# Performance work log

Hardware: AMD Instinct MI355X
Metric: run time of the kernel (lower is better)

Reference implementation:

```python
import jax, jax.numpy as jnp
import numpy as np
from jax import lax


def setup_inputs() -> dict:
    key = jax.random.key(0)
    ks = jax.random.split(key, 6)
    B, C, H, W = 8, 128, 64, 64   # C = 2*channel, channel (per-branch) c = 64
    c = C // 2
    return {
        "x_up": jax.random.normal(ks[0], (B, C, H, W), dtype=jnp.float32),
        "x_skip": jax.random.normal(ks[1], (B, C, H, W), dtype=jnp.float32),
        # nn.Linear(c, 2c): weight [out,in], bias [out]
        "kv1_w": jax.random.normal(ks[2], (2 * c, c), dtype=jnp.float32) * 0.05,
        "kv1_b": jnp.zeros((2 * c,), dtype=jnp.float32),
        "kv2_w": jax.random.normal(ks[3], (2 * c, c), dtype=jnp.float32) * 0.05,
        "kv2_b": jnp.zeros((2 * c,), dtype=jnp.float32),
        # Conv2d(2c, 2c, 3, stride 1, pad 1, bias=False), OIHW
        "conv_w": jax.random.normal(ks[4], (C, C, 3, 3), dtype=jnp.float32) * 0.05,
        # BatchNorm2d(2c) in inference form (running stats)
        "bn_gamma": jax.random.normal(ks[5], (C,), dtype=jnp.float32) * 0.1 + 1.0,
        "bn_beta": jnp.zeros((C,), dtype=jnp.float32),
        "bn_mean": jnp.zeros((C,), dtype=jnp.float32),
        "bn_var": jnp.ones((C,), dtype=jnp.float32),
    }


def reference(x_up, x_skip, kv1_w, kv1_b, kv2_w, kv2_b, conv_w,
              bn_gamma, bn_beta, bn_mean, bn_var):
    b, C, h, w = x_up.shape
    c = C // 2
    hw = h * w
    up1, up2 = x_up[:, :c], x_up[:, c:]
    sk1, sk2 = x_skip[:, :c], x_skip[:, c:]

    # ---- spatial attention branch (softmax over last axis, hw x hw) ----
    shortcut1 = up1 + sk1
    u1 = up1.reshape(b, c, hw).transpose(0, 2, 1)   # (b, hw, c)
    s1 = sk1.reshape(b, c, hw).transpose(0, 2, 1)   # (b, hw, c)
    kv = s1 @ kv1_w.T + kv1_b                        # (b, hw, 2c)
    k1, v1 = kv[..., :c], kv[..., c:]
    attn = jax.nn.softmax(jnp.einsum('bnc,bmc->bnm', u1, k1), axis=-1)  # (b, hw, hw)
    sout = jnp.einsum('bnm,bmc->bnc', attn, v1)      # (b, hw, c)
    sout = sout.transpose(0, 2, 1).reshape(b, c, h, w) + shortcut1

    # ---- channel attention branch (softmax over dim=1 of the c x c map) ----
    shortcut2 = up2 + sk2
    u2 = up2.reshape(b, c, hw).transpose(0, 2, 1)    # (b, hw, c)
    s2 = sk2.reshape(b, c, hw).transpose(0, 2, 1)
    kv = s2 @ kv2_w.T + kv2_b                        # (b, hw, 2c)
    k2, v2 = kv[..., :c], kv[..., c:]
    A = jax.nn.softmax(jnp.einsum('bnc,bnd->bcd', u2, k2), axis=1)  # (b, c, c)
    cout = jnp.einsum('bnc,bcd->bnd', v2, A)          # (b, hw, c)
    cout = cout.transpose(0, 2, 1).reshape(b, c, h, w) + shortcut2

    # ---- conv + BN (inference) + ReLU ----
    x = jnp.concatenate([sout, cout], axis=1)         # (b, 2c, h, w)
    y = lax.conv_general_dilated(x, conv_w, (1, 1), 'SAME',
                                 dimension_numbers=('NCHW', 'OIHW', 'NCHW'))
    inv = jax.lax.rsqrt(bn_var + 1e-5)
    y = (y - bn_mean[None, :, None, None]) * (inv * bn_gamma)[None, :, None, None] \
        + bn_beta[None, :, None, None]
    return jax.nn.relu(y)
```

## Files before the change

### kernel.cpp

```cpp
#include <hip/hip_runtime.h>
#include <math.h>

#define HW 4096

typedef __attribute__((ext_vector_type(8))) short bh8;
typedef __attribute__((ext_vector_type(4))) float f32x4;
typedef __attribute__((ext_vector_type(2))) unsigned int u32x2;
typedef unsigned int u32;
typedef unsigned short u16;

__device__ __forceinline__ u16 f2bf(float f) {
  union { float f; u32 u; } v; v.f = f;
  u32 u = v.u;
  return (u16)((u + 0x7FFFu + ((u >> 16) & 1u)) >> 16);
}
__device__ __forceinline__ float bf2f(u16 h) {
  union { u32 u; float f; } v; v.u = ((u32)h) << 16;
  return v.f;
}
__device__ __forceinline__ float ubits2f(u32 u) {
  union { u32 u; float f; } v; v.u = u;
  return v.f;
}
__device__ __forceinline__ u32 cvt_pk_bf16(float lo, float hi) {
  u32 r;
  asm("v_cvt_pk_bf16_f32 %0, %1, %2" : "=v"(r) : "v"(lo), "v"(hi));
  return r;
}
__device__ __forceinline__ float fexp2(float x) {
  float r;
  asm("v_exp_f32 %0, %1" : "=v"(r) : "v"(x));
  return r;
}

__global__ __launch_bounds__(256) void kv_proj(
    const float* __restrict__ xs,
    const float* __restrict__ w1, const float* __restrict__ b1,
    const float* __restrict__ w2, const float* __restrict__ b2,
    u32* __restrict__ Knm, u16* __restrict__ Vcm,
    u16* __restrict__ K2t, u16* __restrict__ V2t,
    const float* __restrict__ cw, const float* __restrict__ gamma,
    const float* __restrict__ beta, const float* __restrict__ mean,
    const float* __restrict__ var, u16* __restrict__ Wg,
    float* __restrict__ shb) {
  __shared__ __align__(16) u16 XsH[64][72];
  __shared__ __align__(16) u16 XsL[64][72];
  __shared__ u32 LtK[64][33];
  const int b = blockIdx.y, n0 = blockIdx.x * 64;
  const int t = threadIdx.x;
  const int wq = t >> 6, lane = t & 63, lq = lane & 15, quad = lane >> 4;
  const float* xsb = xs + (size_t)b * 128 * HW;

  {
    int gid = (blockIdx.y * 64 + blockIdx.x) * 256 + t;
    for (int i = gid; i < 147456; i += 131072) {
      int tap = i >> 14, oc = (i >> 7) & 127, ic = i & 127;
      float sc = gamma[oc] * rsqrtf(var[oc] + 1e-5f);
      Wg[i] = f2bf(cw[((size_t)(oc * 128 + ic)) * 9 + tap] * sc);
    }
    if (gid < 128) {
      float sc = gamma[gid] * rsqrtf(var[gid] + 1e-5f);
      shb[gid] = beta[gid] - mean[gid] * sc;
    }
  }

  for (int br = 0; br < 2; ++br) {
    const float* W = br ? w2 : w1;
    const float* bias = br ? b2 : b1;
    const float* src = xsb + (br ? 64 * HW : 0);

    bh8 wh[2][2], wl[2][2];
#pragma unroll
    for (int jt = 0; jt < 2; ++jt)
#pragma unroll
      for (int s = 0; s < 2; ++s) {
        const float* wr = W + (size_t)(wq * 32 + jt * 16 + lq) * 64 + s * 32 + quad * 8;
        float4 a0 = *(const float4*)wr;
        float4 a1 = *(const float4*)(wr + 4);
        float f[8] = {a0.x, a0.y, a0.z, a0.w, a1.x, a1.y, a1.z, a1.w};
        union { u32 u[4]; bh8 v; } H, L;
#pragma unroll
        for (int p = 0; p < 4; ++p) {
          u32 hp = cvt_pk_bf16(f[2 * p], f[2 * p + 1]);
          float h0 = ubits2f(hp << 16);
          float h1 = ubits2f(hp & 0xFFFF0000u);
          H.u[p] = hp;
          L.u[p] = cvt_pk_bf16(f[2 * p] - h0, f[2 * p + 1] - h1);
        }
        wh[jt][s] = H.v;
        wl[jt][s] = L.v;
      }

    if (br) __syncthreads();
    {
      const int n = t & 63, cg = t >> 6;
#pragma unroll
      for (int s8 = 0; s8 < 8; ++s8) {
        int ch0 = s8 * 8 + cg * 2;
        float f0 = src[(size_t)ch0 * HW + n0 + n];
        float f1 = src[(size_t)(ch0 + 1) * HW + n0 + n];
        u32 hp = cvt_pk_bf16(f0, f1);
        float h0 = ubits2f(hp << 16);
        float h1 = ubits2f(hp & 0xFFFF0000u);
        u32 lp = cvt_pk_bf16(f0 - h0, f1 - h1);
        *(u32*)&XsH[n][ch0] = hp;
        *(u32*)&XsL[n][ch0] = lp;
      }
    }
    __syncthreads();

    f32x4 acc[2][4];
#pragma unroll
    for (int nt = 0; nt < 4; ++nt) {
      const int xr = nt * 16 + lq;
      bh8 xh0 = *(const bh8*)&XsH[xr][quad * 8];
      bh8 xh1 = *(const bh8*)&XsH[xr][32 + quad * 8];
      bh8 xl0 = *(const bh8*)&XsL[xr][quad * 8];
      bh8 xl1 = *(const bh8*)&XsL[xr][32 + quad * 8];
#pragma unroll
      for (int jt = 0; jt < 2; ++jt) {
        f32x4 a = (f32x4)(0.f);
        a = __builtin_amdgcn_mfma_f32_16x16x32_bf16(wh[jt][0], xh0, a, 0, 0, 0);
        a = __builtin_amdgcn_mfma_f32_16x16x32_bf16(wh[jt][1], xh1, a, 0, 0, 0);
        a = __builtin_amdgcn_mfma_f32_16x16x32_bf16(wh[jt][0], xl0, a, 0, 0, 0);
        a = __builtin_amdgcn_mfma_f32_16x16x32_bf16(wh[jt][1], xl1, a, 0, 0, 0);
        a = __builtin_amdgcn_mfma_f32_16x16x32_bf16(wl[jt][0], xh0, a, 0, 0, 0);
        a = __builtin_amdgcn_mfma_f32_16x16x32_bf16(wl[jt][1], xh1, a, 0, 0, 0);
        acc[jt][nt] = a;
      }
    }

    if (br == 0) {
      if (wq < 2) {
#pragma unroll
        for (int jt = 0; jt < 2; ++jt) {
          float4 bv = *(const float4*)&bias[wq * 32 + jt * 16 + quad * 4];
#pragma unroll
          for (int nt = 0; nt < 4; ++nt) {
            f32x4 a = acc[jt][nt];
            LtK[nt * 16 + lq][wq * 16 + jt * 8 + quad * 2] =
                cvt_pk_bf16(a[0] + bv.x, a[1] + bv.y);
            LtK[nt * 16 + lq][wq * 16 + jt * 8 + quad * 2 + 1] =
                cvt_pk_bf16(a[2] + bv.z, a[3] + bv.w);
          }
        }
      } else {
#pragma unroll
        for (int jt = 0; jt < 2; ++jt) {
          float4 bv = *(const float4*)&bias[wq * 32 + jt * 16 + quad * 4];
          float bvv[4] = {bv.x, bv.y, bv.z, bv.w};
#pragma unroll
          for (int nt = 0; nt < 4; ++nt)
#pragma unroll
            for (int r = 0; r < 4; ++r) {
              int ch = (wq - 2) * 32 + jt * 16 + quad * 4 + r;
              Vcm[((size_t)b * 64 + ch) * HW + n0 + nt * 16 + lq] =
                  f2bf(acc[jt][nt][r] + bvv[r]);
            }
        }
      }
      __syncthreads();
#pragma unroll
      for (int p = 0; p < 8; ++p) {
        int idx = p * 256 + t;
        int n = idx >> 5, cc = idx & 31;
        Knm[((size_t)b * HW + n0 + n) * 32 + cc] = LtK[n][cc];
      }
    } else {
      u16* base = (wq < 2) ? (K2t + (size_t)b * 64 * HW) : (V2t + (size_t)b * 64 * HW);
      const int chb = (wq & 1) * 32;
#pragma unroll
      for (int jt = 0; jt < 2; ++jt) {
        float4 bv = *(const float4*)&bias[wq * 32 + jt * 16 + quad * 4];
        float bvv[4] = {bv.x, bv.y, bv.z, bv.w};
#pragma unroll
        for (int nt = 0; nt < 4; ++nt)
#pragma unroll
          for (int r = 0; r < 4; ++r) {
            int ch = chb + jt * 16 + quad * 4 + r;
            base[(size_t)ch * HW + n0 + nt * 16 + lq] =
                f2bf(acc[jt][nt][r] + bvv[r]);
          }
      }
    }
  }
}

__device__ __forceinline__ void attn_step(
    const bh8* kf, const bh8* vf, const bh8 (&qb)[4][2], const bh8 ones,
    f32x4 (&O)[4][4], f32x4 (&Osum)[4]) {
  f32x4 S[2][4];
  __builtin_amdgcn_s_setprio(1);
#pragma unroll
  for (int mt = 0; mt < 2; ++mt)
#pragma unroll
    for (int nt = 0; nt < 4; ++nt) {
      f32x4 a = (f32x4)(0.f);
      a = __builtin_amdgcn_mfma_f32_16x16x32_bf16(kf[mt * 2 + 0], qb[nt][0], a, 0, 0, 0);
      a = __builtin_amdgcn_mfma_f32_16x16x32_bf16(kf[mt * 2 + 1], qb[nt][1], a, 0, 0, 0);
      S[mt][nt] = a;
    }
  __builtin_amdgcn_s_setprio(0);
#pragma unroll
  for (int nt = 0; nt < 4; ++nt) {
    const float c = 17.312340f;
    float e00 = fexp2(S[0][nt][0] - c), e01 = fexp2(S[0][nt][1] - c);
    float e02 = fexp2(S[0][nt][2] - c), e03 = fexp2(S[0][nt][3] - c);
    float e10 = fexp2(S[1][nt][0] - c), e11 = fexp2(S[1][nt][1] - c);
    float e12 = fexp2(S[1][nt][2] - c), e13 = fexp2(S[1][nt][3] - c);
    u32 A = cvt_pk_bf16(e00, e01);
    u32 B = cvt_pk_bf16(e02, e03);
    u32 C = cvt_pk_bf16(e10, e11);
    u32 D = cvt_pk_bf16(e12, e13);
    u32x2 rac = __builtin_amdgcn_permlane32_swap(A, C, 0, 0);
    u32x2 rbd = __builtin_amdgcn_permlane32_swap(B, D, 0, 0);
    u32x2 r02 = __builtin_amdgcn_permlane16_swap(rac.x, rac.y, 0, 0);
    u32x2 r13 = __builtin_amdgcn_permlane16_swap(rbd.x, rbd.y, 0, 0);
    union { u32 u[4]; bh8 v; } pb;
    pb.u[0] = r02.x;
    pb.u[1] = r13.x;
    pb.u[2] = r02.y;
    pb.u[3] = r13.y;
    __builtin_amdgcn_s_setprio(1);
#pragma unroll
    for (int ct = 0; ct < 4; ++ct)
      O[ct][nt] = __builtin_amdgcn_mfma_f32_16x16x32_bf16(vf[ct], pb.v, O[ct][nt], 0, 0, 0);
    Osum[nt] = __builtin_amdgcn_mfma_f32_16x16x32_bf16(ones, pb.v, Osum[nt], 0, 0, 0);
    __builtin_amdgcn_s_setprio(0);
  }
}

#define LOADKV(KB, KF, VF)                                            \
  do {                                                                \
    const int n0_ = (KB) * 128;                                       \
    const u16* kr_ = Kb + (size_t)(n0_ + wb + lq) * 64 + quad * 8;    \
    KF[0] = *(const bh8*)(kr_);                                       \
    KF[1] = *(const bh8*)(kr_ + 32);                                  \
    KF[2] = *(const bh8*)(kr_ + 1024);                                \
    KF[3] = *(const bh8*)(kr_ + 1056);                                \
    const u16* vr_ = Vb + (size_t)lq * HW + n0_ + wb + quad * 8;      \
    VF[0] = *(const bh8*)(vr_);                                       \
    VF[1] = *(const bh8*)(vr_ + 16 * HW);                             \
    VF[2] = *(const bh8*)(vr_ + 32 * HW);                             \
    VF[3] = *(const bh8*)(vr_ + 48 * HW);                             \
  } while (0)

__global__ __launch_bounds__(256, 2) void attn_gram(
    const float* __restrict__ xu, const float* __restrict__ xs,
    const u16* __restrict__ Knm, const u16* __restrict__ Vcm,
    u16* __restrict__ xcat,
    const u16* __restrict__ K2t, float* __restrict__ Mp) {
  __shared__ __align__(16) u16 SMEM[18432];
  const int b = blockIdx.y;
  const int t = threadIdx.x;

  if (blockIdx.x >= 64) {
    float* Us = (float*)SMEM;
    float* Ksm = Us + 64 * 65;
    const int n0 = (blockIdx.x - 64) * 128;
    const int c = t & 63, dg = t >> 6;
    const float* ub = xu + ((size_t)b * 128 + 64) * HW;
    const u16* kb2 = K2t + (size_t)b * 64 * HW;
    float acc[16];
#pragma unroll
    for (int i = 0; i < 16; ++i) acc[i] = 0.f;
    for (int s = 0; s < 2; ++s) {
      int nn = n0 + s * 64;
      __syncthreads();
      for (int r = 0; r < 16; ++r) {
        int row = r * 4 + dg;
        Us[row * 65 + c] = ub[(size_t)row * HW + nn + c];
        Ksm[row * 65 + c] = bf2f(kb2[(size_t)row * HW + nn + c]);
      }
      __syncthreads();
      for (int n = 0; n < 64; ++n) {
        float u = Us[c * 65 + n];
#pragma unroll
        for (int i = 0; i < 16; ++i)
          acc[i] = fmaf(Ksm[(dg * 16 + i) * 65 + n], u, acc[i]);
      }
    }
    float* dst = Mp + ((size_t)(blockIdx.x - 64) * 8 + b) * 4096 + c * 64 + dg * 16;
#pragma unroll
    for (int i = 0; i < 16; ++i) dst[i] = acc[i];
    return;
  }

  const int q0 = blockIdx.x * 64;
  const int wq = t >> 6, lane = t & 63, lq = lane & 15, quad = lane >> 4;
  const int wb = wq * 32;
  const float* xub = xu + (size_t)b * 128 * HW;
  const float* xsb = xs + (size_t)b * 128 * HW;
  const u16* Kb = Knm + (size_t)b * HW * 64;
  const u16* Vb = Vcm + (size_t)b * 64 * HW;

  bh8 qb[4][2];
#pragma unroll
  for (int nt = 0; nt < 4; ++nt)
#pragma unroll
    for (int s = 0; s < 2; ++s)
#pragma unroll
      for (int j = 0; j < 8; ++j) {
        int ch = s * 32 + quad * 8 + j;
        qb[nt][s][j] =
            (short)f2bf(xub[(size_t)ch * HW + q0 + nt * 16 + lq] * 1.44269504f);
      }
  bh8 ones;
#pragma unroll
  for (int j = 0; j < 8; ++j) ones[j] = (short)0x3F80;

  f32x4 O[4][4];
#pragma unroll
  for (int ct = 0; ct < 4; ++ct)
#pragma unroll
    for (int nt = 0; nt < 4; ++nt) O[ct][nt] = (f32x4)(0.f);
  f32x4 Osum[4];
#pragma unroll
  for (int nt = 0; nt < 4; ++nt) Osum[nt] = (f32x4)(0.f);

  bh8 kfa[4], vfa[4], kfb[4], vfb[4];
  LOADKV(0, kfa, vfa);
  for (int kb = 0; kb < 32; kb += 2) {
    LOADKV(kb + 1, kfb, vfb);
    attn_step(kfa, vfa, qb, ones, O, Osum);
    if (kb + 2 < 32) LOADKV(kb + 2, kfa, vfa);
    attn_step(kfb, vfb, qb, ones, O, Osum);
  }

  float* Posc = (float*)SMEM;
  float* Lred = (float*)(SMEM + 17408);
  if (quad == 0) {
#pragma unroll
    for (int nt = 0; nt < 4; ++nt) Lred[(wq * 4 + nt) * 16 + lq] = Osum[nt][0];
  }

  const int q = t & 63, cg = t >> 6;
#pragma unroll
  for (int rh = 0; rh < 2; ++rh) {
    if (rh) __syncthreads();
#pragma unroll
    for (int c2 = 0; c2 < 2; ++c2)
#pragma unroll
      for (int nt = 0; nt < 4; ++nt)
#pragma unroll
        for (int r = 0; r < 4; ++r)
          Posc[(wq * 32 + c2 * 16 + quad * 4 + r) * 68 + nt * 16 + lq] =
              O[rh * 2 + c2][nt][r];
    __syncthreads();
    float li = 0.f;
#pragma unroll
    for (int w2 = 0; w2 < 4; ++w2) li += Lred[w2 * 64 + q];
    float inv = 1.f / li;
    u16 h[8];
#pragma unroll
    for (int i = 0; i < 8; ++i) {
      int chl = cg * 8 + i;
      float s = 0.f;
#pragma unroll
      for (int w2 = 0; w2 < 4; ++w2) s += Posc[(w2 * 32 + chl) * 68 + q];
      int ch = rh * 32 + chl;
      size_t g = (size_t)ch * HW + q0 + q;
      h[i] = f2bf(s * inv + xub[g] + xsb[g]);
    }
    u32 pk[4];
#pragma unroll
    for (int j = 0; j < 4; ++j) pk[j] = (u32)h[2 * j] | ((u32)h[2 * j + 1] << 16);
    u16* ob = xcat + ((size_t)b * HW + q0 + q) * 128 + rh * 32 + cg * 8;
    *(uint4*)ob = make_uint4(pk[0], pk[1], pk[2], pk[3]);
  }
}

__global__ void chan_reduce(const float* __restrict__ Mp, float* __restrict__ M) {
  int idx = blockIdx.x * 256 + threadIdx.x;
  float s = 0.f;
  for (int ch = 0; ch < 32; ++ch) s += Mp[(size_t)ch * 32768 + idx];
  M[idx] = s;
}

__global__ __launch_bounds__(256) void chan_apply(
    const u16* __restrict__ V2t, const float* __restrict__ M,
    const float* __restrict__ xu, const float* __restrict__ xs,
    u16* __restrict__ xcat) {
  __shared__ float Vsm[64][65];
  __shared__ float As[64][65];
  __shared__ float red1[4][64], red2[4][64];
  const int b = blockIdx.y, n0 = blockIdx.x * 64, t = threadIdx.x;
  const int lane = t & 63, dg = t >> 6;
  const u16* Vb = V2t + (size_t)b * 64 * HW;
  for (int s = 0; s < 16; ++s) {
    int c = s * 4 + dg;
    Vsm[lane][c] = bf2f(Vb[(size_t)c * HW + n0 + lane]);
  }
  for (int idx = t; idx < 4096; idx += 256) As[idx >> 6][idx & 63] = M[b * 4096 + idx];
  __syncthreads();
  float mx = -1e30f;
#pragma unroll
  for (int i = 0; i < 16; ++i) mx = fmaxf(mx, As[dg * 16 + i][lane]);
  red1[dg][lane] = mx;
  __syncthreads();
  mx = fmaxf(fmaxf(red1[0][lane], red1[1][lane]), fmaxf(red1[2][lane], red1[3][lane]));
  float se = 0.f;
#pragma unroll
  for (int i = 0; i < 16; ++i) {
    float e = __expf(As[dg * 16 + i][lane] - mx);
    As[dg * 16 + i][lane] = e;
    se += e;
  }
  red2[dg][lane] = se;
  __syncthreads();

  float acc[16];
#pragma unroll
  for (int i = 0; i < 16; ++i) acc[i] = 0.f;
  for (int c = 0; c < 64; ++c) {
    float v = Vsm[lane][c];
#pragma unroll
    for (int i = 0; i < 16; ++i) acc[i] = fmaf(v, As[c][dg * 16 + i], acc[i]);
  }
  const float* xub = xu + ((size_t)b * 128 + 64) * HW;
  const float* xsb = xs + ((size_t)b * 128 + 64) * HW;
  const int n = n0 + lane;
  u16 hv[16];
#pragma unroll
  for (int i = 0; i < 16; ++i) {
    int d = dg * 16 + i;
    float sm = red2[0][d] + red2[1][d] + red2[2][d] + red2[3][d];
    hv[i] = f2bf(acc[i] / sm + xub[(size_t)d * HW + n] + xsb[(size_t)d * HW + n]);
  }
  u32 pk[8];
#pragma unroll
  for (int j = 0; j < 8; ++j) pk[j] = (u32)hv[2 * j] | ((u32)hv[2 * j + 1] << 16);
  u16* ob = xcat + ((size_t)b * HW + n) * 128 + 64 + dg * 16;
  *(uint4*)(ob) = make_uint4(pk[0], pk[1], pk[2], pk[3]);
  *(uint4*)(ob + 8) = make_uint4(pk[4], pk[5], pk[6], pk[7]);
}

__global__ __launch_bounds__(512) void conv_mfma(
    const u16* __restrict__ X, const u16* __restrict__ Wg,
    const float* __restrict__ shb, float* __restrict__ out) {
  __shared__ __align__(16) u16 In[4 * 66 * 136];
  __shared__ __align__(16) u16 Wt[2][128 * 136];
  const int b = blockIdx.y, h0 = blockIdx.x * 2;
  const int t = threadIdx.x;
  const int wq = t >> 6, lane = t & 63, lq = lane & 15, quad = lane >> 4;
  const int nb = (wq & 1) * 64;
  const int mb = (wq >> 1) * 2;
  const u16* Xb = X + (size_t)b * HW * 128;

  if (t < 128) {
    int ih = t >> 5, iwsel = (t >> 4) & 1, ck = t & 15;
    int iw = iwsel ? 65 : 0;
    *(uint4*)&In[(ih * 66 + iw) * 136 + ck * 8] = make_uint4(0, 0, 0, 0);
  }
  for (int ih = 0; ih < 4; ++ih) {
    int h = h0 - 1 + ih;
    bool ok = (h >= 0 && h < 64);
    const u16* src = Xb + (size_t)h * 64 * 128;
#pragma unroll
    for (int p = 0; p < 2; ++p) {
      int idx = p * 512 + t;
      int row = idx >> 4, ck = idx & 15;
      uint4 d = make_uint4(0, 0, 0, 0);
      if (ok) d = *(const uint4*)(src + (size_t)row * 128 + ck * 8);
      *(uint4*)&In[(ih * 66 + 1 + row) * 136 + ck * 8] = d;
    }
  }
  {
    const u16* src = Wg;
#pragma unroll
    for (int p = 0; p < 4; ++p) {
      int idx = p * 512 + t;
      int oc = idx >> 4, ck = idx & 15;
      uint4 d = *(const uint4*)(src + oc * 128 + ck * 8);
      *(uint4*)&Wt[0][oc * 136 + ck * 8] = d;
    }
  }
  __syncthreads();

  f32x4 acc[2][4];
#pragma unroll
  for (int mt = 0; mt < 2; ++mt)
#pragma unroll
    for (int nt = 0; nt < 4; ++nt) acc[mt][nt] = (f32x4)(0.f);

  for (int tap = 0; tap < 9; ++tap) {
    const int cur = tap & 1;
    if (tap < 8) {
      const u16* src = Wg + (size_t)(tap + 1) * 128 * 128;
#pragma unroll
      for (int p = 0; p < 4; ++p) {
        int idx = p * 512 + t;
        int oc = idx >> 4, ck = idx & 15;
        uint4 d = *(const uint4*)(src + oc * 128 + ck * 8);
        *(uint4*)&Wt[cur ^ 1][oc * 136 + ck * 8] = d;
      }
    }
    const int dh = tap / 3, dw = tap - 3 * dh;
    const u16* Wc = &Wt[cur][0];
#pragma unroll
    for (int c = 0; c < 4; ++c) {
      bh8 bf[4];
#pragma unroll
      for (int nt = 0; nt < 4; ++nt)
        bf[nt] = *(const bh8*)&Wc[(nb + nt * 16 + lq) * 136 + c * 32 + quad * 8];
#pragma unroll
      for (int mt = 0; mt < 2; ++mt) {
        int s = (mb + mt) * 16 + lq;
        int ih = (s >> 6) + dh, iw = (s & 63) + dw;
        bh8 af = *(const bh8*)&In[(ih * 66 + iw) * 136 + c * 32 + quad * 8];
#pragma unroll
        for (int nt = 0; nt < 4; ++nt)
          acc[mt][nt] = __builtin_amdgcn_mfma_f32_16x16x32_bf16(af, bf[nt], acc[mt][nt], 0, 0, 0);
      }
    }
    __syncthreads();
  }

  float shv[4];
#pragma unroll
  for (int nt = 0; nt < 4; ++nt) shv[nt] = shb[nb + nt * 16 + lq];
#pragma unroll
  for (int mt = 0; mt < 2; ++mt) {
    int mtile = mb + mt;
    int h = h0 + (mtile >> 2);
    int w0 = ((mtile & 3) * 16) + quad * 4;
#pragma unroll
    for (int nt = 0; nt < 4; ++nt) {
      int oc = nb + nt * 16 + lq;
      float4 v;
      v.x = fmaxf(acc[mt][nt][0] + shv[nt], 0.f);
      v.y = fmaxf(acc[mt][nt][1] + shv[nt], 0.f);
      v.z = fmaxf(acc[mt][nt][2] + shv[nt], 0.f);
      v.w = fmaxf(acc[mt][nt][3] + shv[nt], 0.f);
      *(float4*)&out[((size_t)b * 128 + oc) * HW + h * 64 + w0] = v;
    }
  }
}

extern "C" void kernel_launch(void* const* d_in, const int* in_sizes, int n_in,
                              void* d_out, int out_size, void* d_ws, size_t ws_size,
                              hipStream_t stream) {
  const float* x_up   = (const float*)d_in[0];
  const float* x_skip = (const float*)d_in[1];
  const float* kv1_w  = (const float*)d_in[2];
  const float* kv1_b  = (const float*)d_in[3];
  const float* kv2_w  = (const float*)d_in[4];
  const float* kv2_b  = (const float*)d_in[5];
  const float* conv_w = (const float*)d_in[6];
  const float* bn_g   = (const float*)d_in[7];
  const float* bn_b   = (const float*)d_in[8];
  const float* bn_m   = (const float*)d_in[9];
  const float* bn_v   = (const float*)d_in[10];
  float* out = (float*)d_out;

  char* ws = (char*)d_ws;
  const size_t XCATB_B = (size_t)8 * HW * 128 * 2;
  const size_t KV16_B  = (size_t)8 * 64 * HW * 2;
  size_t off = 0;
  u16*   xcat = (u16*)(ws + off);   off += XCATB_B;
  u16*   K2t  = (u16*)(ws + off);   off += KV16_B;
  u16*   V2t  = (u16*)(ws + off);   off += KV16_B;
  u32*   Knm  = (u32*)(ws + off);   off += KV16_B;
  u16*   Vcm  = (u16*)(ws + off);   off += KV16_B;
  float* Mp   = (float*)(ws + off); off += (size_t)32 * 8 * 4096 * 4;
  float* M    = (float*)(ws + off); off += (size_t)8 * 4096 * 4;
  u16*   Wg   = (u16*)(ws + off);   off += (size_t)9 * 128 * 128 * 2;
  float* shb  = (float*)(ws + off); off += 512;

  kv_proj<<<dim3(64, 8), 256, 0, stream>>>(x_skip, kv1_w, kv1_b, kv2_w, kv2_b,
                                           Knm, Vcm, K2t, V2t,
                                           conv_w, bn_g, bn_b, bn_m, bn_v, Wg, shb);
  attn_gram<<<dim3(96, 8), 256, 0, stream>>>(x_up, x_skip, (const u16*)Knm, Vcm,
                                             xcat, K2t, Mp);
  chan_reduce<<<128, 256, 0, stream>>>(Mp, M);
  chan_apply<<<dim3(64, 8), 256, 0, stream>>>(V2t, M, x_up, x_skip, xcat);
  conv_mfma<<<dim3(32, 8), 512, 0, stream>>>(xcat, Wg, shb, out);
}
```

Baseline: 212.7 us.

## Software-pipeline QK/softmax-PV, MFMA gram blocks with atomics, drop reduce kernel

The attention main loop is split into separate QK and softmax/PV steps, so the QK MFMAs for the next key block are issued before the exp/PV work of the current block, letting matrix and VALU work overlap. The channel Gram-matrix blocks switch from scalar FMA over shared memory to bf16 MFMA with a hi/lo split of the fp32 activations. They accumulate straight into M with atomicAdd, which removes the partial buffer and the chan_reduce launch. M is zeroed in kv_proj. The cost is more live registers (two S tiles), atomic contention, and a non-deterministic summation order.

```diff
diff --git a/kernel.cpp b/kernel.cpp
--- a/kernel.cpp
+++ b/kernel.cpp
@@ -42,7 +42,7 @@
     const float* __restrict__ cw, const float* __restrict__ gamma,
     const float* __restrict__ beta, const float* __restrict__ mean,
     const float* __restrict__ var, u16* __restrict__ Wg,
-    float* __restrict__ shb) {
+    float* __restrict__ shb, float* __restrict__ M) {
   __shared__ __align__(16) u16 XsH[64][72];
   __shared__ __align__(16) u16 XsL[64][72];
   __shared__ u32 LtK[64][33];
@@ -62,6 +62,7 @@
       float sc = gamma[gid] * rsqrtf(var[gid] + 1e-5f);
       shb[gid] = beta[gid] - mean[gid] * sc;
     }
+    if (gid < 32768) M[gid] = 0.f;
   }
 
   for (int br = 0; br < 2; ++br) {
@@ -186,10 +187,8 @@
   }
 }
 
-__device__ __forceinline__ void attn_step(
-    const bh8* kf, const bh8* vf, const bh8 (&qb)[4][2], const bh8 ones,
-    f32x4 (&O)[4][4], f32x4 (&Osum)[4]) {
-  f32x4 S[2][4];
+__device__ __forceinline__ void qk_step(
+    const bh8* kf, const bh8 (&qb)[4][2], f32x4 (&S)[2][4]) {
   __builtin_amdgcn_s_setprio(1);
 #pragma unroll
   for (int mt = 0; mt < 2; ++mt)
@@ -201,6 +200,11 @@
       S[mt][nt] = a;
     }
   __builtin_amdgcn_s_setprio(0);
+}
+
+__device__ __forceinline__ void sm_pv(
+    const f32x4 (&S)[2][4], const bh8* vf, const bh8 ones,
+    f32x4 (&O)[4][4], f32x4 (&Osum)[4]) {
 #pragma unroll
   for (int nt = 0; nt < 4; ++nt) {
     const float c = 17.312340f;
@@ -249,45 +253,53 @@
     const float* __restrict__ xu, const float* __restrict__ xs,
     const u16* __restrict__ Knm, const u16* __restrict__ Vcm,
     u16* __restrict__ xcat,
-    const u16* __restrict__ K2t, float* __restrict__ Mp) {
+    const u16* __restrict__ K2t, float* __restrict__ M) {
   __shared__ __align__(16) u16 SMEM[18432];
   const int b = blockIdx.y;
   const int t = threadIdx.x;
+  const int wq = t >> 6, lane = t & 63, lq = lane & 15, quad = lane >> 4;
 
   if (blockIdx.x >= 64) {
-    float* Us = (float*)SMEM;
-    float* Ksm = Us + 64 * 65;
-    const int n0 = (blockIdx.x - 64) * 128;
-    const int c = t & 63, dg = t >> 6;
+    const int chunk = blockIdx.x - 64;
+    const int nn = chunk * 128;
     const float* ub = xu + ((size_t)b * 128 + 64) * HW;
     const u16* kb2 = K2t + (size_t)b * 64 * HW;
-    float acc[16];
-#pragma unroll
-    for (int i = 0; i < 16; ++i) acc[i] = 0.f;
-    for (int s = 0; s < 2; ++s) {
-      int nn = n0 + s * 64;
-      __syncthreads();
-      for (int r = 0; r < 16; ++r) {
-        int row = r * 4 + dg;
-        Us[row * 65 + c] = ub[(size_t)row * HW + nn + c];
-        Ksm[row * 65 + c] = bf2f(kb2[(size_t)row * HW + nn + c]);
-      }
-      __syncthreads();
-      for (int n = 0; n < 64; ++n) {
-        float u = Us[c * 65 + n];
-#pragma unroll
-        for (int i = 0; i < 16; ++i)
-          acc[i] = fmaf(Ksm[(dg * 16 + i) * 65 + n], u, acc[i]);
-      }
-    }
-    float* dst = Mp + ((size_t)(blockIdx.x - 64) * 8 + b) * 4096 + c * 64 + dg * 16;
-#pragma unroll
-    for (int i = 0; i < 16; ++i) dst[i] = acc[i];
+    f32x4 acc[4];
+#pragma unroll
+    for (int ct = 0; ct < 4; ++ct) acc[ct] = (f32x4)(0.f);
+#pragma unroll
+    for (int kc = 0; kc < 4; ++kc) {
+      const int nb2 = nn + kc * 32 + quad * 8;
+      bh8 kb_ = *(const bh8*)&kb2[(size_t)(wq * 16 + lq) * HW + nb2];
+#pragma unroll
+      for (int ct = 0; ct < 4; ++ct) {
+        const float* ar = ub + (size_t)(ct * 16 + lq) * HW + nb2;
+        float4 a0 = *(const float4*)ar;
+        float4 a1 = *(const float4*)(ar + 4);
+        float f[8] = {a0.x, a0.y, a0.z, a0.w, a1.x, a1.y, a1.z, a1.w};
+        union { u32 u[4]; bh8 v; } H, L;
+#pragma unroll
+        for (int p = 0; p < 4; ++p) {
+          u32 hp = cvt_pk_bf16(f[2 * p], f[2 * p + 1]);
+          float h0 = ubits2f(hp << 16);
+          float h1 = ubits2f(hp & 0xFFFF0000u);
+          H.u[p] = hp;
+          L.u[p] = cvt_pk_bf16(f[2 * p] - h0, f[2 * p + 1] - h1);
+        }
+        acc[ct] = __builtin_amdgcn_mfma_f32_16x16x32_bf16(H.v, kb_, acc[ct], 0, 0, 0);
+        acc[ct] = __builtin_amdgcn_mfma_f32_16x16x32_bf16(L.v, kb_, acc[ct], 0, 0, 0);
+      }
+    }
+    float* Mb = M + (size_t)b * 4096;
+#pragma unroll
+    for (int ct = 0; ct < 4; ++ct)
+#pragma unroll
+      for (int r = 0; r < 4; ++r)
+        atomicAdd(&Mb[(ct * 16 + quad * 4 + r) * 64 + wq * 16 + lq], acc[ct][r]);
     return;
   }
 
   const int q0 = blockIdx.x * 64;
-  const int wq = t >> 6, lane = t & 63, lq = lane & 15, quad = lane >> 4;
   const int wb = wq * 32;
   const float* xub = xu + (size_t)b * 128 * HW;
   const float* xsb = xs + (size_t)b * 128 * HW;
@@ -319,12 +331,19 @@
   for (int nt = 0; nt < 4; ++nt) Osum[nt] = (f32x4)(0.f);
 
   bh8 kfa[4], vfa[4], kfb[4], vfb[4];
+  f32x4 Sa[2][4], Sb[2][4];
   LOADKV(0, kfa, vfa);
+  qk_step(kfa, qb, Sa);
+  LOADKV(1, kfb, vfb);
   for (int kb = 0; kb < 32; kb += 2) {
-    LOADKV(kb + 1, kfb, vfb);
-    attn_step(kfa, vfa, qb, ones, O, Osum);
-    if (kb + 2 < 32) LOADKV(kb + 2, kfa, vfa);
-    attn_step(kfb, vfb, qb, ones, O, Osum);
+    qk_step(kfb, qb, Sb);
+    sm_pv(Sa, vfa, ones, O, Osum);
+    if (kb + 2 < 32) {
+      LOADKV(kb + 2, kfa, vfa);
+      qk_step(kfa, qb, Sa);
+    }
+    sm_pv(Sb, vfb, ones, O, Osum);
+    if (kb + 3 < 32) LOADKV(kb + 3, kfb, vfb);
   }
 
   float* Posc = (float*)SMEM;
@@ -368,13 +387,6 @@
     u16* ob = xcat + ((size_t)b * HW + q0 + q) * 128 + rh * 32 + cg * 8;
     *(uint4*)ob = make_uint4(pk[0], pk[1], pk[2], pk[3]);
   }
-}
-
-__global__ void chan_reduce(const float* __restrict__ Mp, float* __restrict__ M) {
-  int idx = blockIdx.x * 256 + threadIdx.x;
-  float s = 0.f;
-  for (int ch = 0; ch < 32; ++ch) s += Mp[(size_t)ch * 32768 + idx];
-  M[idx] = s;
 }
 
 __global__ __launch_bounds__(256) void chan_apply(
@@ -562,17 +574,16 @@
   u16*   V2t  = (u16*)(ws + off);   off += KV16_B;
   u32*   Knm  = (u32*)(ws + off);   off += KV16_B;
   u16*   Vcm  = (u16*)(ws + off);   off += KV16_B;
-  float* Mp   = (float*)(ws + off); off += (size_t)32 * 8 * 4096 * 4;
   float* M    = (float*)(ws + off); off += (size_t)8 * 4096 * 4;
   u16*   Wg   = (u16*)(ws + off);   off += (size_t)9 * 128 * 128 * 2;
   float* shb  = (float*)(ws + off); off += 512;
 
   kv_proj<<<dim3(64, 8), 256, 0, stream>>>(x_skip, kv1_w, kv1_b, kv2_w, kv2_b,
                                            Knm, Vcm, K2t, V2t,
-                                           conv_w, bn_g, bn_b, bn_m, bn_v, Wg, shb);
+                                           conv_w, bn_g, bn_b, bn_m, bn_v, Wg,
+                                           shb, M);
   attn_gram<<<dim3(96, 8), 256, 0, stream>>>(x_up, x_skip, (const u16*)Knm, Vcm,
-                                             xcat, K2t, Mp);
-  chan_reduce<<<128, 256, 0, stream>>>(Mp, M);
+                                             xcat, K2t, M);
   chan_apply<<<dim3(64, 8), 256, 0, stream>>>(V2t, M, x_up, x_skip, xcat);
   conv_mfma<<<dim3(32, 8), 512, 0, stream>>>(xcat, Wg, shb, out);
 }
```

Result: no change. 215.8 us (+1.5%).
